# Kernel optimization log

Measured on AMD Instinct MI355X. Metric: run time of the kernel, lower is better.

The kernel has to match this reference:

```python
import jax, jax.numpy as jnp
import numpy as np

N, E = 100000, 1600000
IN, HID, OUT = 128, 64, 64
BN_EPS = 1e-5


def setup_inputs() -> dict:
    key = jax.random.key(0)
    ks = jax.random.split(key, 6)
    x = jax.random.normal(ks[0], (N, IN), dtype=jnp.float32)
    edge_index = jax.random.randint(ks[1], (2, E), 0, N, dtype=jnp.int32)
    W1 = jax.random.normal(ks[2], (IN, HID), dtype=jnp.float32) / np.sqrt(IN).astype(np.float32)
    b1 = jnp.zeros((HID,), jnp.float32)
    bn_weight = jnp.ones((HID,), jnp.float32)
    bn_bias = jnp.zeros((HID,), jnp.float32)
    W2 = jax.random.normal(ks[3], (HID, OUT), dtype=jnp.float32) / np.sqrt(HID).astype(np.float32)
    b2 = jnp.zeros((OUT,), jnp.float32)
    return {"x": x, "edge_index": edge_index, "W1": W1, "b1": b1,
            "bn_weight": bn_weight, "bn_bias": bn_bias, "W2": W2, "b2": b2}


def _gcn_conv(x, W, b, src, dst, deg_inv_sqrt):
    # PyG GCNConv: linear first, then symmetric-normalized aggregation with self-loops.
    h = x @ W                                        # [N, out]
    norm = deg_inv_sqrt[src] * deg_inv_sqrt[dst]     # [E]
    agg = jax.ops.segment_sum(h[src] * norm[:, None], dst, num_segments=h.shape[0])
    # self-loop contribution: norm = 1/deg
    agg = agg + h * (deg_inv_sqrt * deg_inv_sqrt)[:, None]
    return agg + b


def reference(x, edge_index, W1, b1, bn_weight, bn_bias, W2, b2):
    src, dst = edge_index[0], edge_index[1]
    # degree including self-loop (GCNConv add_self_loops=True, edge_weight=1)
    deg = jax.ops.segment_sum(jnp.ones((E,), x.dtype), dst, num_segments=N) + 1.0
    deg_inv_sqrt = jax.lax.rsqrt(deg)
    h = _gcn_conv(x, W1, b1, src, dst, deg_inv_sqrt)
    # BatchNorm1d (training-mode batch statistics, biased variance)
    mean = jnp.mean(h, axis=0)
    var = jnp.var(h, axis=0)
    h = (h - mean) * jax.lax.rsqrt(var + BN_EPS) * bn_weight + bn_bias
    h = jax.nn.relu(h)
    # dropout: inference mode (identity)
    return _gcn_conv(h, W2, b2, src, dst, deg_inv_sqrt)
```

## Files before the change

### kernel.cpp

```cpp
#include <hip/hip_runtime.h>

#define N_NODES 100000
#define E_EDGES 1600000
#define IN_F    128
#define HID_F   64
#define OUT_F   64
#define BN_EPS  1e-5f
#define NBUK    391
#define CHUNK   6250
#define NGBLK   3125
#define NMBLK   1563

typedef __bf16 bf16x8 __attribute__((ext_vector_type(8)));
typedef float  f32x4  __attribute__((ext_vector_type(4)));

__device__ __forceinline__ float bflo(unsigned int u) { return __uint_as_float(u << 16); }
__device__ __forceinline__ float bfhi(unsigned int u) { return __uint_as_float(u & 0xFFFF0000u); }
__device__ __forceinline__ unsigned int pack2bf(float a, float b) {
    unsigned int ua = __float_as_uint(a), ub = __float_as_uint(b);
    ua = (ua + 0x7fffu + ((ua >> 16) & 1u)) >> 16;
    ub = (ub + 0x7fffu + ((ub >> 16) & 1u)) >> 16;
    return ua | (ub << 16);
}
__device__ __forceinline__ unsigned short bf1(float a) {
    unsigned int ua = __float_as_uint(a);
    return (unsigned short)((ua + 0x7fffu + ((ua >> 16) & 1u)) >> 16);
}
#define ADD8(A, u)                                           \
    do {                                                     \
        A[0] += bflo((u).x); A[1] += bfhi((u).x);            \
        A[2] += bflo((u).y); A[3] += bfhi((u).y);            \
        A[4] += bflo((u).z); A[5] += bfhi((u).z);            \
        A[6] += bflo((u).w); A[7] += bfhi((u).w);            \
    } while (0)

__global__ __launch_bounds__(512) void k_chist(const int* __restrict__ dstv,
                                               int* __restrict__ histbuf) {
    __shared__ int h[NBUK];
    const int tid = threadIdx.x;
    const int e0 = blockIdx.x * CHUNK;
    for (int b = tid; b < NBUK; b += 512) h[b] = 0;
    __syncthreads();
    for (int t = tid; t < CHUNK; t += 512)
        atomicAdd(&h[dstv[e0 + t] >> 8], 1);
    __syncthreads();
    for (int b = tid; b < NBUK; b += 512)
        histbuf[blockIdx.x * NBUK + b] = h[b];
}

__global__ __launch_bounds__(512) void k_cscan(const int* __restrict__ histbuf,
                                               int* __restrict__ coff,
                                               int* __restrict__ ccur) {
    __shared__ int sh[512];
    const int tid = threadIdx.x;
    int v = 0;
    if (tid < NBUK)
        for (int b = 0; b < 256; ++b) v += histbuf[b * NBUK + tid];
    sh[tid] = v;
    __syncthreads();
    for (int off = 1; off < 512; off <<= 1) {
        int t = (tid >= off) ? sh[tid - off] : 0;
        __syncthreads();
        sh[tid] += t;
        __syncthreads();
    }
    int excl = sh[tid] - v;
    if (tid < NBUK) { coff[tid] = excl; ccur[tid] = excl; }
    if (tid == 0) coff[NBUK] = E_EDGES;
}

__global__ __launch_bounds__(512) void k_bucket(const int* __restrict__ srcv,
                                                const int* __restrict__ dstv,
                                                int* __restrict__ ccur,
                                                unsigned int* __restrict__ aux) {
    __shared__ int dl[CHUNK];
    __shared__ int hist[NBUK], base[NBUK], lcur[NBUK];
    const int tid = threadIdx.x;
    const int e0 = blockIdx.x * CHUNK;
    for (int b = tid; b < NBUK; b += 512) hist[b] = 0;
    __syncthreads();
    for (int t = tid; t < CHUNK; t += 512) {
        int d = dstv[e0 + t];
        dl[t] = d;
        atomicAdd(&hist[d >> 8], 1);
    }
    __syncthreads();
    for (int b = tid; b < NBUK; b += 512) {
        int h = hist[b];
        if (h) base[b] = atomicAdd(&ccur[b], h);
        lcur[b] = 0;
    }
    __syncthreads();
    for (int t = tid; t < CHUNK; t += 512) {
        int d = dl[t];
        int b = d >> 8;
        int off = atomicAdd(&lcur[b], 1);
        aux[base[b] + off] = ((unsigned int)srcv[e0 + t] << 8) | (unsigned int)(d & 255);
    }
}

__global__ __launch_bounds__(256) void k_csrnode(const int* __restrict__ coff,
                                                 const unsigned int* __restrict__ aux,
                                                 int* __restrict__ rowptr,
                                                 float* __restrict__ dis,
                                                 int* __restrict__ csr_src) {
    __shared__ int c0[256], sc[256], cur[256];
    const int tid = threadIdx.x;
    const int n0 = blockIdx.x * 256;
    const int nn = min(256, N_NODES - n0);
    const int estart = coff[blockIdx.x];
    const int eend   = coff[blockIdx.x + 1];
    c0[tid] = 0;
    __syncthreads();
    for (int e = estart + tid; e < eend; e += 256)
        atomicAdd(&c0[aux[e] & 255], 1);
    __syncthreads();
    int v = c0[tid];
    sc[tid] = v;
    __syncthreads();
    for (int off = 1; off < 256; off <<= 1) {
        int t = (tid >= off) ? sc[tid - off] : 0;
        __syncthreads();
        sc[tid] += t;
        __syncthreads();
    }
    int excl = sc[tid] - v;
    if (tid < nn) {
        int p = estart + excl;
        rowptr[n0 + tid] = p;
        cur[tid] = p;
        dis[n0 + tid] = rsqrtf((float)v + 1.0f);
    }
    if (blockIdx.x == NBUK - 1 && tid == 0) rowptr[N_NODES] = E_EDGES;
    __syncthreads();
    for (int e = estart + tid; e < eend; e += 256) {
        unsigned int u = aux[e];
        int pos = atomicAdd(&cur[u & 255], 1);
        csr_src[pos] = (int)(u >> 8);
    }
}

__global__ __launch_bounds__(256) void k_gemm1(const float* __restrict__ x,
                                               const float* __restrict__ W1,
                                               const float* __restrict__ dis,
                                               unsigned short* __restrict__ hs1) {
    __shared__ unsigned short Asb[64 * 136];
    __shared__ unsigned short Btb[64 * 136];
    __shared__ unsigned short Cc[64 * 72];
    __shared__ float disS[64];
    const int tid = threadIdx.x;
    const int r0 = blockIdx.x * 64;

    if (tid < 64) disS[tid] = (r0 + tid < N_NODES) ? dis[r0 + tid] : 0.f;

    const float4* x4 = (const float4*)x;
#pragma unroll
    for (int p = 0; p < 4; ++p) {
        int idx8 = p * 256 + tid;
        int row = idx8 >> 4, c8 = idx8 & 15;
        float4 v0 = make_float4(0.f, 0.f, 0.f, 0.f), v1 = v0;
        if (r0 + row < N_NODES) {
            v0 = x4[(size_t)(r0 + row) * 32 + c8 * 2];
            v1 = x4[(size_t)(r0 + row) * 32 + c8 * 2 + 1];
        }
        uint4 u;
        u.x = pack2bf(v0.x, v0.y); u.y = pack2bf(v0.z, v0.w);
        u.z = pack2bf(v1.x, v1.y); u.w = pack2bf(v1.z, v1.w);
        *(uint4*)&Asb[row * 136 + c8 * 8] = u;
    }
    for (int idx = tid; idx < IN_F * HID_F; idx += 256) {
        int k = idx >> 6, n = idx & 63;
        Btb[n * 136 + k] = bf1(W1[idx]);
    }
    __syncthreads();

    const int wv = tid >> 6, lane = tid & 63;
    const int m = lane & 15, quad = lane >> 4;
    const int arow = wv * 16 + m;
    f32x4 acc[4] = {};
#pragma unroll
    for (int ks = 0; ks < 4; ++ks) {
        int k0 = ks * 32 + quad * 8;
        bf16x8 af = *(const bf16x8*)&Asb[arow * 136 + k0];
#pragma unroll
        for (int c = 0; c < 4; ++c) {
            bf16x8 bfr = *(const bf16x8*)&Btb[(c * 16 + m) * 136 + k0];
            acc[c] = __builtin_amdgcn_mfma_f32_16x16x32_bf16(af, bfr, acc[c], 0, 0, 0);
        }
    }
#pragma unroll
    for (int c = 0; c < 4; ++c)
#pragma unroll
        for (int r = 0; r < 4; ++r) {
            int rl = wv * 16 + quad * 4 + r;
            Cc[rl * 72 + c * 16 + m] = bf1(acc[c][r] * disS[rl]);
        }
    __syncthreads();
#pragma unroll
    for (int p = 0; p < 2; ++p) {
        int idx = p * 256 + tid;
        int row = idx >> 3, c8 = idx & 7;
        if (r0 + row < N_NODES)
            *(uint4*)&hs1[(size_t)(r0 + row) * 64 + c8 * 8] = *(uint4*)&Cc[row * 72 + c8 * 8];
    }
}

__global__ __launch_bounds__(256) void k_gather1(const int* __restrict__ rowptr,
                                                 const int* __restrict__ csr_src,
                                                 const unsigned short* __restrict__ hsb,
                                                 const float* __restrict__ dis,
                                                 const float* __restrict__ b1,
                                                 unsigned short* __restrict__ aggb,
                                                 float* __restrict__ partials) {
    const int tid = threadIdx.x;
    const int g = tid >> 3, q = tid & 7;
    const int n = blockIdx.x * 32 + g;
    const uint4* __restrict__ hs16 = (const uint4*)hsb;

    const int start = rowptr[n], end = rowptr[n + 1];
    float A0[8] = {}, A1[8] = {}, A2[8] = {}, A3[8] = {};
    {
        uint4 u = hs16[(size_t)n * 8 + q];
        ADD8(A0, u);
    }
    int i = start;
    for (; i + 7 < end; i += 8) {
        int s0 = csr_src[i + 0], s1 = csr_src[i + 1];
        int s2 = csr_src[i + 2], s3 = csr_src[i + 3];
        int s4 = csr_src[i + 4], s5 = csr_src[i + 5];
        int s6 = csr_src[i + 6], s7 = csr_src[i + 7];
        uint4 u0 = hs16[(size_t)s0 * 8 + q];
        uint4 u1 = hs16[(size_t)s1 * 8 + q];
        uint4 u2 = hs16[(size_t)s2 * 8 + q];
        uint4 u3 = hs16[(size_t)s3 * 8 + q];
        uint4 u4 = hs16[(size_t)s4 * 8 + q];
        uint4 u5 = hs16[(size_t)s5 * 8 + q];
        uint4 u6 = hs16[(size_t)s6 * 8 + q];
        uint4 u7 = hs16[(size_t)s7 * 8 + q];
        ADD8(A0, u0); ADD8(A1, u1); ADD8(A2, u2); ADD8(A3, u3);
        ADD8(A0, u4); ADD8(A1, u5); ADD8(A2, u6); ADD8(A3, u7);
    }
    if (i + 3 < end) {
        int s0 = csr_src[i + 0], s1 = csr_src[i + 1];
        int s2 = csr_src[i + 2], s3 = csr_src[i + 3];
        uint4 u0 = hs16[(size_t)s0 * 8 + q];
        uint4 u1 = hs16[(size_t)s1 * 8 + q];
        uint4 u2 = hs16[(size_t)s2 * 8 + q];
        uint4 u3 = hs16[(size_t)s3 * 8 + q];
        ADD8(A0, u0); ADD8(A1, u1); ADD8(A2, u2); ADD8(A3, u3);
        i += 4;
    }
    for (; i < end; ++i) {
        uint4 u = hs16[(size_t)csr_src[i] * 8 + q];
        ADD8(A0, u);
    }
    const float d = dis[n];
    const float4 blo = ((const float4*)b1)[q * 2];
    const float4 bhi = ((const float4*)b1)[q * 2 + 1];
    float o[8];
    o[0] = fmaf(d, A0[0] + A1[0] + A2[0] + A3[0], blo.x);
    o[1] = fmaf(d, A0[1] + A1[1] + A2[1] + A3[1], blo.y);
    o[2] = fmaf(d, A0[2] + A1[2] + A2[2] + A3[2], blo.z);
    o[3] = fmaf(d, A0[3] + A1[3] + A2[3] + A3[3], blo.w);
    o[4] = fmaf(d, A0[4] + A1[4] + A2[4] + A3[4], bhi.x);
    o[5] = fmaf(d, A0[5] + A1[5] + A2[5] + A3[5], bhi.y);
    o[6] = fmaf(d, A0[6] + A1[6] + A2[6] + A3[6], bhi.z);
    o[7] = fmaf(d, A0[7] + A1[7] + A2[7] + A3[7], bhi.w);
    uint4 ob;
    ob.x = pack2bf(o[0], o[1]); ob.y = pack2bf(o[2], o[3]);
    ob.z = pack2bf(o[4], o[5]); ob.w = pack2bf(o[6], o[7]);
    ((uint4*)aggb)[(size_t)n * 8 + q] = ob;

    __shared__ float4 redA[256], redB[256];
    redA[tid] = make_float4(o[0], o[1], o[2], o[3]);
    redB[tid] = make_float4(o[4], o[5], o[6], o[7]);
    __syncthreads();
    for (int s = 128; s >= 8; s >>= 1) {
        if (tid < s) {
            redA[tid].x += redA[tid + s].x; redA[tid].y += redA[tid + s].y;
            redA[tid].z += redA[tid + s].z; redA[tid].w += redA[tid + s].w;
            redB[tid].x += redB[tid + s].x; redB[tid].y += redB[tid + s].y;
            redB[tid].z += redB[tid + s].z; redB[tid].w += redB[tid + s].w;
        }
        __syncthreads();
    }
    float4* pr = (float4*)(partials + (size_t)blockIdx.x * 128);
    if (tid < 8) { pr[tid * 2] = redA[tid]; pr[tid * 2 + 1] = redB[tid]; }
    __syncthreads();
    redA[tid] = make_float4(o[0] * o[0], o[1] * o[1], o[2] * o[2], o[3] * o[3]);
    redB[tid] = make_float4(o[4] * o[4], o[5] * o[5], o[6] * o[6], o[7] * o[7]);
    __syncthreads();
    for (int s = 128; s >= 8; s >>= 1) {
        if (tid < s) {
            redA[tid].x += redA[tid + s].x; redA[tid].y += redA[tid + s].y;
            redA[tid].z += redA[tid + s].z; redA[tid].w += redA[tid + s].w;
            redB[tid].x += redB[tid + s].x; redB[tid].y += redB[tid + s].y;
            redB[tid].z += redB[tid + s].z; redB[tid].w += redB[tid + s].w;
        }
        __syncthreads();
    }
    if (tid < 8) { pr[16 + tid * 2] = redA[tid]; pr[16 + tid * 2 + 1] = redB[tid]; }
}

__global__ __launch_bounds__(256) void k_bnfinal(const float* __restrict__ partials,
                                                 float* __restrict__ bnstats) {
    const int c = blockIdx.x;
    const int tid = threadIdx.x;
    float s = 0.f;
    for (int r = tid; r < NGBLK; r += 256)
        s += partials[(size_t)r * 128 + c];
    __shared__ float sh[256];
    sh[tid] = s;
    __syncthreads();
    for (int st = 128; st > 0; st >>= 1) {
        if (tid < st) sh[tid] += sh[tid + st];
        __syncthreads();
    }
    if (tid == 0) bnstats[c] = sh[0];
}

__global__ __launch_bounds__(256) void k_gemm2(const unsigned short* __restrict__ aggb,
                                               const float* __restrict__ W2,
                                               const float* __restrict__ dis,
                                               const float* __restrict__ bnw,
                                               const float* __restrict__ bnb,
                                               const float* __restrict__ bnstats,
                                               unsigned short* __restrict__ hs2) {
    __shared__ unsigned short Ab[64 * 72];
    __shared__ unsigned short Bt2[64 * 72];
    __shared__ unsigned short Cc[64 * 72];
    __shared__ float scale_s[64], shift_s[64], disS[64];
    const int tid = threadIdx.x;
    const int r0 = blockIdx.x * 64;

    if (tid < 64) {
        const float invN = 1.0f / (float)N_NODES;
        float mean = bnstats[tid] * invN;
        float var  = bnstats[64 + tid] * invN - mean * mean;
        float sc   = bnw[tid] * rsqrtf(var + BN_EPS);
        scale_s[tid] = sc;
        shift_s[tid] = fmaf(-mean, sc, bnb[tid]);
        disS[tid] = (r0 + tid < N_NODES) ? dis[r0 + tid] : 0.f;
    }
    for (int idx = tid; idx < HID_F * OUT_F; idx += 256) {
        int k = idx >> 6, n = idx & 63;
        Bt2[n * 72 + k] = bf1(W2[idx]);
    }
    __syncthreads();

    const uint4* a16 = (const uint4*)aggb;
#pragma unroll
    for (int p = 0; p < 2; ++p) {
        int idx = p * 256 + tid;
        int row = idx >> 3, q = idx & 7;
        uint4 u = make_uint4(0, 0, 0, 0);
        if (r0 + row < N_NODES) u = a16[(size_t)(r0 + row) * 8 + q];
        int k0 = q * 8;
        float v[8];
        v[0] = bflo(u.x); v[1] = bfhi(u.x); v[2] = bflo(u.y); v[3] = bfhi(u.y);
        v[4] = bflo(u.z); v[5] = bfhi(u.z); v[6] = bflo(u.w); v[7] = bfhi(u.w);
        uint4 o;
        float w0 = fmaxf(fmaf(v[0], scale_s[k0 + 0], shift_s[k0 + 0]), 0.f);
        float w1 = fmaxf(fmaf(v[1], scale_s[k0 + 1], shift_s[k0 + 1]), 0.f);
        float w2 = fmaxf(fmaf(v[2], scale_s[k0 + 2], shift_s[k0 + 2]), 0.f);
        float w3 = fmaxf(fmaf(v[3], scale_s[k0 + 3], shift_s[k0 + 3]), 0.f);
        float w4 = fmaxf(fmaf(v[4], scale_s[k0 + 4], shift_s[k0 + 4]), 0.f);
        float w5 = fmaxf(fmaf(v[5], scale_s[k0 + 5], shift_s[k0 + 5]), 0.f);
        float w6 = fmaxf(fmaf(v[6], scale_s[k0 + 6], shift_s[k0 + 6]), 0.f);
        float w7 = fmaxf(fmaf(v[7], scale_s[k0 + 7], shift_s[k0 + 7]), 0.f);
        o.x = pack2bf(w0, w1); o.y = pack2bf(w2, w3);
        o.z = pack2bf(w4, w5); o.w = pack2bf(w6, w7);
        *(uint4*)&Ab[row * 72 + q * 8] = o;
    }
    __syncthreads();

    const int wv = tid >> 6, lane = tid & 63;
    const int m = lane & 15, quad = lane >> 4;
    const int arow = wv * 16 + m;
    f32x4 acc[4] = {};
#pragma unroll
    for (int ks = 0; ks < 2; ++ks) {
        int k0 = ks * 32 + quad * 8;
        bf16x8 af = *(const bf16x8*)&Ab[arow * 72 + k0];
#pragma unroll
        for (int c = 0; c < 4; ++c) {
            bf16x8 bfr = *(const bf16x8*)&Bt2[(c * 16 + m) * 72 + k0];
            acc[c] = __builtin_amdgcn_mfma_f32_16x16x32_bf16(af, bfr, acc[c], 0, 0, 0);
        }
    }
#pragma unroll
    for (int c = 0; c < 4; ++c)
#pragma unroll
        for (int r = 0; r < 4; ++r) {
            int rl = wv * 16 + quad * 4 + r;
            Cc[rl * 72 + c * 16 + m] = bf1(acc[c][r] * disS[rl]);
        }
    __syncthreads();
#pragma unroll
    for (int p = 0; p < 2; ++p) {
        int idx = p * 256 + tid;
        int row = idx >> 3, c8 = idx & 7;
        if (r0 + row < N_NODES)
            *(uint4*)&hs2[(size_t)(r0 + row) * 64 + c8 * 8] = *(uint4*)&Cc[row * 72 + c8 * 8];
    }
}

__global__ __launch_bounds__(256) void k_gather2(const int* __restrict__ rowptr,
                                                 const int* __restrict__ csr_src,
                                                 const unsigned short* __restrict__ hsb,
                                                 const float* __restrict__ dis,
                                                 const float* __restrict__ b2,
                                                 float* __restrict__ out) {
    const int tid = threadIdx.x;
    const int g = tid >> 3, q = tid & 7;
    const int n = blockIdx.x * 32 + g;
    const uint4* __restrict__ hs16 = (const uint4*)hsb;

    const int start = rowptr[n], end = rowptr[n + 1];
    float A0[8] = {}, A1[8] = {}, A2[8] = {}, A3[8] = {};
    {
        uint4 u = hs16[(size_t)n * 8 + q];
        ADD8(A0, u);
    }
    int i = start;
    for (; i + 7 < end; i += 8) {
        int s0 = csr_src[i + 0], s1 = csr_src[i + 1];
        int s2 = csr_src[i + 2], s3 = csr_src[i + 3];
        int s4 = csr_src[i + 4], s5 = csr_src[i + 5];
        int s6 = csr_src[i + 6], s7 = csr_src[i + 7];
        uint4 u0 = hs16[(size_t)s0 * 8 + q];
        uint4 u1 = hs16[(size_t)s1 * 8 + q];
        uint4 u2 = hs16[(size_t)s2 * 8 + q];
        uint4 u3 = hs16[(size_t)s3 * 8 + q];
        uint4 u4 = hs16[(size_t)s4 * 8 + q];
        uint4 u5 = hs16[(size_t)s5 * 8 + q];
        uint4 u6 = hs16[(size_t)s6 * 8 + q];
        uint4 u7 = hs16[(size_t)s7 * 8 + q];
        ADD8(A0, u0); ADD8(A1, u1); ADD8(A2, u2); ADD8(A3, u3);
        ADD8(A0, u4); ADD8(A1, u5); ADD8(A2, u6); ADD8(A3, u7);
    }
    if (i + 3 < end) {
        int s0 = csr_src[i + 0], s1 = csr_src[i + 1];
        int s2 = csr_src[i + 2], s3 = csr_src[i + 3];
        uint4 u0 = hs16[(size_t)s0 * 8 + q];
        uint4 u1 = hs16[(size_t)s1 * 8 + q];
        uint4 u2 = hs16[(size_t)s2 * 8 + q];
        uint4 u3 = hs16[(size_t)s3 * 8 + q];
        ADD8(A0, u0); ADD8(A1, u1); ADD8(A2, u2); ADD8(A3, u3);
        i += 4;
    }
    for (; i < end; ++i) {
        uint4 u = hs16[(size_t)csr_src[i] * 8 + q];
        ADD8(A0, u);
    }
    const float d = dis[n];
    const float4 blo = ((const float4*)b2)[q * 2];
    const float4 bhi = ((const float4*)b2)[q * 2 + 1];
    float4 o0, o1;
    o0.x = fmaf(d, A0[0] + A1[0] + A2[0] + A3[0], blo.x);
    o0.y = fmaf(d, A0[1] + A1[1] + A2[1] + A3[1], blo.y);
    o0.z = fmaf(d, A0[2] + A1[2] + A2[2] + A3[2], blo.z);
    o0.w = fmaf(d, A0[3] + A1[3] + A2[3] + A3[3], blo.w);
    o1.x = fmaf(d, A0[4] + A1[4] + A2[4] + A3[4], bhi.x);
    o1.y = fmaf(d, A0[5] + A1[5] + A2[5] + A3[5], bhi.y);
    o1.z = fmaf(d, A0[6] + A1[6] + A2[6] + A3[6], bhi.z);
    o1.w = fmaf(d, A0[7] + A1[7] + A2[7] + A3[7], bhi.w);
    float4* op = (float4*)(out + (size_t)n * OUT_F + q * 8);
    op[0] = o0;
    op[1] = o1;
}

extern "C" void kernel_launch(void* const* d_in, const int* in_sizes, int n_in,
                              void* d_out, int out_size, void* d_ws, size_t ws_size,
                              hipStream_t stream) {
    const float* x   = (const float*)d_in[0];
    const int*   ei  = (const int*)d_in[1];
    const float* W1  = (const float*)d_in[2];
    const float* b1  = (const float*)d_in[3];
    const float* bnw = (const float*)d_in[4];
    const float* bnb = (const float*)d_in[5];
    const float* W2  = (const float*)d_in[6];
    const float* b2  = (const float*)d_in[7];
    float* out = (float*)d_out;

    float* ws = (float*)d_ws;
    float*        dis     = ws;
    int*          rowptr  = (int*)(ws + 100352);
    int*          coff    = (int*)(ws + 200960);
    int*          ccur    = (int*)(ws + 201472);
    float*        bnstats = ws + 201984;
    int*          histbuf = (int*)(ws + 202112);
    int*          csr_src = (int*)(ws + 302464);
    float*        bufA    = ws + 1902464;
    float*        bufB    = bufA + (size_t)N_NODES * HID_F;
    unsigned int*   aux  = (unsigned int*)bufA;
    unsigned short* hsb  = (unsigned short*)bufA;
    unsigned short* aggb = (unsigned short*)bufB;
    float* partials = out;

    const int* srcv = ei;
    const int* dstv = ei + E_EDGES;

    k_chist  <<<256, 512, 0, stream>>>(dstv, histbuf);
    k_cscan  <<<1, 512, 0, stream>>>(histbuf, coff, ccur);
    k_bucket <<<256, 512, 0, stream>>>(srcv, dstv, ccur, aux);
    k_csrnode<<<NBUK, 256, 0, stream>>>(coff, aux, rowptr, dis, csr_src);

    k_gemm1  <<<NMBLK, 256, 0, stream>>>(x, W1, dis, hsb);
    k_gather1<<<NGBLK, 256, 0, stream>>>(rowptr, csr_src, hsb, dis, b1, aggb, partials);
    k_bnfinal<<<128, 256, 0, stream>>>(partials, bnstats);
    k_gemm2  <<<NMBLK, 256, 0, stream>>>(aggb, W2, dis, bnw, bnb, bnstats, hsb);
    k_gather2<<<NGBLK, 256, 0, stream>>>(rowptr, csr_src, hsb, dis, b2, out);
}
```

Measured before the change: 252.0 us.

## Parallelize bucket scan and process four nodes per group in gather kernels

The single-block column-sum scan is replaced by a per-bucket parallel scan over the 256 chunk histograms plus a small scan of bucket totals. This yields deterministic per-chunk write offsets, so the bucketing kernel drops its second shared-memory histogram pass and its global atomics. The gather kernels now use 64-thread blocks, with each 8-lane group handling four nodes in sequence, and BN partial statistics are accumulated in registers before the block reduction. The cost is less parallelism per block in the gathers and one extra kernel launch.

New measurement: 239.8 us. 4.9% less time.

```diff
diff --git a/kernel.cpp b/kernel.cpp
--- a/kernel.cpp
+++ b/kernel.cpp
@@ -48,14 +48,28 @@
         histbuf[blockIdx.x * NBUK + b] = h[b];
 }
 
-__global__ __launch_bounds__(512) void k_cscan(const int* __restrict__ histbuf,
-                                               int* __restrict__ coff,
-                                               int* __restrict__ ccur) {
+__global__ __launch_bounds__(256) void k_cscan1(int* __restrict__ histbuf,
+                                                int* __restrict__ btot) {
+    __shared__ int sh[256];
+    const int bkt = blockIdx.x, tid = threadIdx.x;
+    int v = histbuf[tid * NBUK + bkt];
+    sh[tid] = v;
+    __syncthreads();
+    for (int off = 1; off < 256; off <<= 1) {
+        int t = (tid >= off) ? sh[tid - off] : 0;
+        __syncthreads();
+        sh[tid] += t;
+        __syncthreads();
+    }
+    histbuf[tid * NBUK + bkt] = sh[tid] - v;
+    if (tid == 255) btot[bkt] = sh[255];
+}
+
+__global__ __launch_bounds__(512) void k_cscan2(const int* __restrict__ btot,
+                                                int* __restrict__ coff) {
     __shared__ int sh[512];
     const int tid = threadIdx.x;
-    int v = 0;
-    if (tid < NBUK)
-        for (int b = 0; b < 256; ++b) v += histbuf[b * NBUK + tid];
+    int v = (tid < NBUK) ? btot[tid] : 0;
     sh[tid] = v;
     __syncthreads();
     for (int off = 1; off < 512; off <<= 1) {
@@ -64,38 +78,26 @@
         sh[tid] += t;
         __syncthreads();
     }
-    int excl = sh[tid] - v;
-    if (tid < NBUK) { coff[tid] = excl; ccur[tid] = excl; }
+    if (tid < NBUK) coff[tid] = sh[tid] - v;
     if (tid == 0) coff[NBUK] = E_EDGES;
 }
 
 __global__ __launch_bounds__(512) void k_bucket(const int* __restrict__ srcv,
                                                 const int* __restrict__ dstv,
-                                                int* __restrict__ ccur,
+                                                const int* __restrict__ histbuf,
+                                                const int* __restrict__ coff,
                                                 unsigned int* __restrict__ aux) {
-    __shared__ int dl[CHUNK];
-    __shared__ int hist[NBUK], base[NBUK], lcur[NBUK];
+    __shared__ int cur[NBUK];
     const int tid = threadIdx.x;
     const int e0 = blockIdx.x * CHUNK;
-    for (int b = tid; b < NBUK; b += 512) hist[b] = 0;
+    for (int i = tid; i < NBUK; i += 512)
+        cur[i] = histbuf[blockIdx.x * NBUK + i] + coff[i];
     __syncthreads();
     for (int t = tid; t < CHUNK; t += 512) {
         int d = dstv[e0 + t];
-        dl[t] = d;
-        atomicAdd(&hist[d >> 8], 1);
-    }
-    __syncthreads();
-    for (int b = tid; b < NBUK; b += 512) {
-        int h = hist[b];
-        if (h) base[b] = atomicAdd(&ccur[b], h);
-        lcur[b] = 0;
-    }
-    __syncthreads();
-    for (int t = tid; t < CHUNK; t += 512) {
-        int d = dl[t];
-        int b = d >> 8;
-        int off = atomicAdd(&lcur[b], 1);
-        aux[base[b] + off] = ((unsigned int)srcv[e0 + t] << 8) | (unsigned int)(d & 255);
+        int s = srcv[e0 + t];
+        int pos = atomicAdd(&cur[d >> 8], 1);
+        aux[pos] = ((unsigned int)s << 8) | (unsigned int)(d & 255);
     }
 }
 
@@ -205,77 +207,88 @@
     }
 }
 
-__global__ __launch_bounds__(256) void k_gather1(const int* __restrict__ rowptr,
-                                                 const int* __restrict__ csr_src,
-                                                 const unsigned short* __restrict__ hsb,
-                                                 const float* __restrict__ dis,
-                                                 const float* __restrict__ b1,
-                                                 unsigned short* __restrict__ aggb,
-                                                 float* __restrict__ partials) {
+__global__ __launch_bounds__(64) void k_gather1(const int* __restrict__ rowptr,
+                                                const int* __restrict__ csr_src,
+                                                const unsigned short* __restrict__ hsb,
+                                                const float* __restrict__ dis,
+                                                const float* __restrict__ b1,
+                                                unsigned short* __restrict__ aggb,
+                                                float* __restrict__ partials) {
     const int tid = threadIdx.x;
     const int g = tid >> 3, q = tid & 7;
-    const int n = blockIdx.x * 32 + g;
     const uint4* __restrict__ hs16 = (const uint4*)hsb;
-
-    const int start = rowptr[n], end = rowptr[n + 1];
-    float A0[8] = {}, A1[8] = {}, A2[8] = {}, A3[8] = {};
-    {
-        uint4 u = hs16[(size_t)n * 8 + q];
-        ADD8(A0, u);
-    }
-    int i = start;
-    for (; i + 7 < end; i += 8) {
-        int s0 = csr_src[i + 0], s1 = csr_src[i + 1];
-        int s2 = csr_src[i + 2], s3 = csr_src[i + 3];
-        int s4 = csr_src[i + 4], s5 = csr_src[i + 5];
-        int s6 = csr_src[i + 6], s7 = csr_src[i + 7];
-        uint4 u0 = hs16[(size_t)s0 * 8 + q];
-        uint4 u1 = hs16[(size_t)s1 * 8 + q];
-        uint4 u2 = hs16[(size_t)s2 * 8 + q];
-        uint4 u3 = hs16[(size_t)s3 * 8 + q];
-        uint4 u4 = hs16[(size_t)s4 * 8 + q];
-        uint4 u5 = hs16[(size_t)s5 * 8 + q];
-        uint4 u6 = hs16[(size_t)s6 * 8 + q];
-        uint4 u7 = hs16[(size_t)s7 * 8 + q];
-        ADD8(A0, u0); ADD8(A1, u1); ADD8(A2, u2); ADD8(A3, u3);
-        ADD8(A0, u4); ADD8(A1, u5); ADD8(A2, u6); ADD8(A3, u7);
-    }
-    if (i + 3 < end) {
-        int s0 = csr_src[i + 0], s1 = csr_src[i + 1];
-        int s2 = csr_src[i + 2], s3 = csr_src[i + 3];
-        uint4 u0 = hs16[(size_t)s0 * 8 + q];
-        uint4 u1 = hs16[(size_t)s1 * 8 + q];
-        uint4 u2 = hs16[(size_t)s2 * 8 + q];
-        uint4 u3 = hs16[(size_t)s3 * 8 + q];
-        ADD8(A0, u0); ADD8(A1, u1); ADD8(A2, u2); ADD8(A3, u3);
-        i += 4;
-    }
-    for (; i < end; ++i) {
-        uint4 u = hs16[(size_t)csr_src[i] * 8 + q];
-        ADD8(A0, u);
-    }
-    const float d = dis[n];
     const float4 blo = ((const float4*)b1)[q * 2];
     const float4 bhi = ((const float4*)b1)[q * 2 + 1];
-    float o[8];
-    o[0] = fmaf(d, A0[0] + A1[0] + A2[0] + A3[0], blo.x);
-    o[1] = fmaf(d, A0[1] + A1[1] + A2[1] + A3[1], blo.y);
-    o[2] = fmaf(d, A0[2] + A1[2] + A2[2] + A3[2], blo.z);
-    o[3] = fmaf(d, A0[3] + A1[3] + A2[3] + A3[3], blo.w);
-    o[4] = fmaf(d, A0[4] + A1[4] + A2[4] + A3[4], bhi.x);
-    o[5] = fmaf(d, A0[5] + A1[5] + A2[5] + A3[5], bhi.y);
-    o[6] = fmaf(d, A0[6] + A1[6] + A2[6] + A3[6], bhi.z);
-    o[7] = fmaf(d, A0[7] + A1[7] + A2[7] + A3[7], bhi.w);
-    uint4 ob;
-    ob.x = pack2bf(o[0], o[1]); ob.y = pack2bf(o[2], o[3]);
-    ob.z = pack2bf(o[4], o[5]); ob.w = pack2bf(o[6], o[7]);
-    ((uint4*)aggb)[(size_t)n * 8 + q] = ob;
-
-    __shared__ float4 redA[256], redB[256];
-    redA[tid] = make_float4(o[0], o[1], o[2], o[3]);
-    redB[tid] = make_float4(o[4], o[5], o[6], o[7]);
-    __syncthreads();
-    for (int s = 128; s >= 8; s >>= 1) {
+
+    float bsA[4] = {}, bsB[4] = {}, bqA[4] = {}, bqB[4] = {};
+
+#pragma unroll
+    for (int jj = 0; jj < 4; ++jj) {
+        const int n = blockIdx.x * 32 + jj * 8 + g;
+        const int start = rowptr[n], end = rowptr[n + 1];
+        float A0[8] = {}, A1[8] = {}, A2[8] = {}, A3[8] = {};
+        {
+            uint4 u = hs16[(size_t)n * 8 + q];
+            ADD8(A0, u);
+        }
+        int i = start;
+        for (; i + 7 < end; i += 8) {
+            int s0 = csr_src[i + 0], s1 = csr_src[i + 1];
+            int s2 = csr_src[i + 2], s3 = csr_src[i + 3];
+            int s4 = csr_src[i + 4], s5 = csr_src[i + 5];
+            int s6 = csr_src[i + 6], s7 = csr_src[i + 7];
+            uint4 u0 = hs16[(size_t)s0 * 8 + q];
+            uint4 u1 = hs16[(size_t)s1 * 8 + q];
+            uint4 u2 = hs16[(size_t)s2 * 8 + q];
+            uint4 u3 = hs16[(size_t)s3 * 8 + q];
+            uint4 u4 = hs16[(size_t)s4 * 8 + q];
+            uint4 u5 = hs16[(size_t)s5 * 8 + q];
+            uint4 u6 = hs16[(size_t)s6 * 8 + q];
+            uint4 u7 = hs16[(size_t)s7 * 8 + q];
+            ADD8(A0, u0); ADD8(A1, u1); ADD8(A2, u2); ADD8(A3, u3);
+            ADD8(A0, u4); ADD8(A1, u5); ADD8(A2, u6); ADD8(A3, u7);
+        }
+        if (i + 3 < end) {
+            int s0 = csr_src[i + 0], s1 = csr_src[i + 1];
+            int s2 = csr_src[i + 2], s3 = csr_src[i + 3];
+            uint4 u0 = hs16[(size_t)s0 * 8 + q];
+            uint4 u1 = hs16[(size_t)s1 * 8 + q];
+            uint4 u2 = hs16[(size_t)s2 * 8 + q];
+            uint4 u3 = hs16[(size_t)s3 * 8 + q];
+            ADD8(A0, u0); ADD8(A1, u1); ADD8(A2, u2); ADD8(A3, u3);
+            i += 4;
+        }
+        for (; i < end; ++i) {
+            uint4 u = hs16[(size_t)csr_src[i] * 8 + q];
+            ADD8(A0, u);
+        }
+        const float d = dis[n];
+        float o[8];
+        o[0] = fmaf(d, A0[0] + A1[0] + A2[0] + A3[0], blo.x);
+        o[1] = fmaf(d, A0[1] + A1[1] + A2[1] + A3[1], blo.y);
+        o[2] = fmaf(d, A0[2] + A1[2] + A2[2] + A3[2], blo.z);
+        o[3] = fmaf(d, A0[3] + A1[3] + A2[3] + A3[3], blo.w);
+        o[4] = fmaf(d, A0[4] + A1[4] + A2[4] + A3[4], bhi.x);
+        o[5] = fmaf(d, A0[5] + A1[5] + A2[5] + A3[5], bhi.y);
+        o[6] = fmaf(d, A0[6] + A1[6] + A2[6] + A3[6], bhi.z);
+        o[7] = fmaf(d, A0[7] + A1[7] + A2[7] + A3[7], bhi.w);
+        uint4 ob;
+        ob.x = pack2bf(o[0], o[1]); ob.y = pack2bf(o[2], o[3]);
+        ob.z = pack2bf(o[4], o[5]); ob.w = pack2bf(o[6], o[7]);
+        ((uint4*)aggb)[(size_t)n * 8 + q] = ob;
+#pragma unroll
+        for (int k = 0; k < 4; ++k) {
+            bsA[k] += o[k];     bsB[k] += o[4 + k];
+            bqA[k] = fmaf(o[k], o[k], bqA[k]);
+            bqB[k] = fmaf(o[4 + k], o[4 + k], bqB[k]);
+        }
+    }
+
+    __shared__ float4 redA[64], redB[64];
+    redA[tid] = make_float4(bsA[0], bsA[1], bsA[2], bsA[3]);
+    redB[tid] = make_float4(bsB[0], bsB[1], bsB[2], bsB[3]);
+    __syncthreads();
+    for (int s = 32; s >= 8; s >>= 1) {
         if (tid < s) {
             redA[tid].x += redA[tid + s].x; redA[tid].y += redA[tid + s].y;
             redA[tid].z += redA[tid + s].z; redA[tid].w += redA[tid + s].w;
@@ -287,10 +300,10 @@
     float4* pr = (float4*)(partials + (size_t)blockIdx.x * 128);
     if (tid < 8) { pr[tid * 2] = redA[tid]; pr[tid * 2 + 1] = redB[tid]; }
     __syncthreads();
-    redA[tid] = make_float4(o[0] * o[0], o[1] * o[1], o[2] * o[2], o[3] * o[3]);
-    redB[tid] = make_float4(o[4] * o[4], o[5] * o[5], o[6] * o[6], o[7] * o[7]);
-    __syncthreads();
-    for (int s = 128; s >= 8; s >>= 1) {
+    redA[tid] = make_float4(bqA[0], bqA[1], bqA[2], bqA[3]);
+    redB[tid] = make_float4(bqB[0], bqB[1], bqB[2], bqB[3]);
+    __syncthreads();
+    for (int s = 32; s >= 8; s >>= 1) {
         if (tid < s) {
             redA[tid].x += redA[tid + s].x; redA[tid].y += redA[tid + s].y;
             redA[tid].z += redA[tid + s].z; redA[tid].w += redA[tid + s].w;
@@ -405,69 +418,72 @@
     }
 }
 
-__global__ __launch_bounds__(256) void k_gather2(const int* __restrict__ rowptr,
-                                                 const int* __restrict__ csr_src,
-                                                 const unsigned short* __restrict__ hsb,
-                                                 const float* __restrict__ dis,
-                                                 const float* __restrict__ b2,
-                                                 float* __restrict__ out) {
+__global__ __launch_bounds__(64) void k_gather2(const int* __restrict__ rowptr,
+                                                const int* __restrict__ csr_src,
+                                                const unsigned short* __restrict__ hsb,
+                                                const float* __restrict__ dis,
+                                                const float* __restrict__ b2,
+                                                float* __restrict__ out) {
     const int tid = threadIdx.x;
     const int g = tid >> 3, q = tid & 7;
-    const int n = blockIdx.x * 32 + g;
     const uint4* __restrict__ hs16 = (const uint4*)hsb;
-
-    const int start = rowptr[n], end = rowptr[n + 1];
-    float A0[8] = {}, A1[8] = {}, A2[8] = {}, A3[8] = {};
-    {
-        uint4 u = hs16[(size_t)n * 8 + q];
-        ADD8(A0, u);
-    }
-    int i = start;
-    for (; i + 7 < end; i += 8) {
-        int s0 = csr_src[i + 0], s1 = csr_src[i + 1];
-        int s2 = csr_src[i + 2], s3 = csr_src[i + 3];
-        int s4 = csr_src[i + 4], s5 = csr_src[i + 5];
-        int s6 = csr_src[i + 6], s7 = csr_src[i + 7];
-        uint4 u0 = hs16[(size_t)s0 * 8 + q];
-        uint4 u1 = hs16[(size_t)s1 * 8 + q];
-        uint4 u2 = hs16[(size_t)s2 * 8 + q];
-        uint4 u3 = hs16[(size_t)s3 * 8 + q];
-        uint4 u4 = hs16[(size_t)s4 * 8 + q];
-        uint4 u5 = hs16[(size_t)s5 * 8 + q];
-        uint4 u6 = hs16[(size_t)s6 * 8 + q];
-        uint4 u7 = hs16[(size_t)s7 * 8 + q];
-        ADD8(A0, u0); ADD8(A1, u1); ADD8(A2, u2); ADD8(A3, u3);
-        ADD8(A0, u4); ADD8(A1, u5); ADD8(A2, u6); ADD8(A3, u7);
-    }
-    if (i + 3 < end) {
-        int s0 = csr_src[i + 0], s1 = csr_src[i + 1];
-        int s2 = csr_src[i + 2], s3 = csr_src[i + 3];
-        uint4 u0 = hs16[(size_t)s0 * 8 + q];
-        uint4 u1 = hs16[(size_t)s1 * 8 + q];
-        uint4 u2 = hs16[(size_t)s2 * 8 + q];
-        uint4 u3 = hs16[(size_t)s3 * 8 + q];
-        ADD8(A0, u0); ADD8(A1, u1); ADD8(A2, u2); ADD8(A3, u3);
-        i += 4;
-    }
-    for (; i < end; ++i) {
-        uint4 u = hs16[(size_t)csr_src[i] * 8 + q];
-        ADD8(A0, u);
-    }
-    const float d = dis[n];
     const float4 blo = ((const float4*)b2)[q * 2];
     const float4 bhi = ((const float4*)b2)[q * 2 + 1];
-    float4 o0, o1;
-    o0.x = fmaf(d, A0[0] + A1[0] + A2[0] + A3[0], blo.x);
-    o0.y = fmaf(d, A0[1] + A1[1] + A2[1] + A3[1], blo.y);
-    o0.z = fmaf(d, A0[2] + A1[2] + A2[2] + A3[2], blo.z);
-    o0.w = fmaf(d, A0[3] + A1[3] + A2[3] + A3[3], blo.w);
-    o1.x = fmaf(d, A0[4] + A1[4] + A2[4] + A3[4], bhi.x);
-    o1.y = fmaf(d, A0[5] + A1[5] + A2[5] + A3[5], bhi.y);
-    o1.z = fmaf(d, A0[6] + A1[6] + A2[6] + A3[6], bhi.z);
-    o1.w = fmaf(d, A0[7] + A1[7] + A2[7] + A3[7], bhi.w);
-    float4* op = (float4*)(out + (size_t)n * OUT_F + q * 8);
-    op[0] = o0;
-    op[1] = o1;
+
+#pragma unroll
+    for (int jj = 0; jj < 4; ++jj) {
+        const int n = blockIdx.x * 32 + jj * 8 + g;
+        const int start = rowptr[n], end = rowptr[n + 1];
+        float A0[8] = {}, A1[8] = {}, A2[8] = {}, A3[8] = {};
+        {
+            uint4 u = hs16[(size_t)n * 8 + q];
+            ADD8(A0, u);
+        }
+        int i = start;
+        for (; i + 7 < end; i += 8) {
+            int s0 = csr_src[i + 0], s1 = csr_src[i + 1];
+            int s2 = csr_src[i + 2], s3 = csr_src[i + 3];
+            int s4 = csr_src[i + 4], s5 = csr_src[i + 5];
+            int s6 = csr_src[i + 6], s7 = csr_src[i + 7];
+            uint4 u0 = hs16[(size_t)s0 * 8 + q];
+            uint4 u1 = hs16[(size_t)s1 * 8 + q];
+            uint4 u2 = hs16[(size_t)s2 * 8 + q];
+            uint4 u3 = hs16[(size_t)s3 * 8 + q];
+            uint4 u4 = hs16[(size_t)s4 * 8 + q];
+            uint4 u5 = hs16[(size_t)s5 * 8 + q];
+            uint4 u6 = hs16[(size_t)s6 * 8 + q];
+            uint4 u7 = hs16[(size_t)s7 * 8 + q];
+            ADD8(A0, u0); ADD8(A1, u1); ADD8(A2, u2); ADD8(A3, u3);
+            ADD8(A0, u4); ADD8(A1, u5); ADD8(A2, u6); ADD8(A3, u7);
+        }
+        if (i + 3 < end) {
+            int s0 = csr_src[i + 0], s1 = csr_src[i + 1];
+            int s2 = csr_src[i + 2], s3 = csr_src[i + 3];
+            uint4 u0 = hs16[(size_t)s0 * 8 + q];
+            uint4 u1 = hs16[(size_t)s1 * 8 + q];
+            uint4 u2 = hs16[(size_t)s2 * 8 + q];
+            uint4 u3 = hs16[(size_t)s3 * 8 + q];
+            ADD8(A0, u0); ADD8(A1, u1); ADD8(A2, u2); ADD8(A3, u3);
+            i += 4;
+        }
+        for (; i < end; ++i) {
+            uint4 u = hs16[(size_t)csr_src[i] * 8 + q];
+            ADD8(A0, u);
+        }
+        const float d = dis[n];
+        float4 o0, o1;
+        o0.x = fmaf(d, A0[0] + A1[0] + A2[0] + A3[0], blo.x);
+        o0.y = fmaf(d, A0[1] + A1[1] + A2[1] + A3[1], blo.y);
+        o0.z = fmaf(d, A0[2] + A1[2] + A2[2] + A3[2], blo.z);
+        o0.w = fmaf(d, A0[3] + A1[3] + A2[3] + A3[3], blo.w);
+        o1.x = fmaf(d, A0[4] + A1[4] + A2[4] + A3[4], bhi.x);
+        o1.y = fmaf(d, A0[5] + A1[5] + A2[5] + A3[5], bhi.y);
+        o1.z = fmaf(d, A0[6] + A1[6] + A2[6] + A3[6], bhi.z);
+        o1.w = fmaf(d, A0[7] + A1[7] + A2[7] + A3[7], bhi.w);
+        float4* op = (float4*)(out + (size_t)n * OUT_F + q * 8);
+        op[0] = o0;
+        op[1] = o1;
+    }
 }
 
 extern "C" void kernel_launch(void* const* d_in, const int* in_sizes, int n_in,
@@ -487,7 +503,7 @@
     float*        dis     = ws;
     int*          rowptr  = (int*)(ws + 100352);
     int*          coff    = (int*)(ws + 200960);
-    int*          ccur    = (int*)(ws + 201472);
+    int*          btot    = (int*)(ws + 201472);
     float*        bnstats = ws + 201984;
     int*          histbuf = (int*)(ws + 202112);
     int*          csr_src = (int*)(ws + 302464);
@@ -502,13 +518,14 @@
     const int* dstv = ei + E_EDGES;
 
     k_chist  <<<256, 512, 0, stream>>>(dstv, histbuf);
-    k_cscan  <<<1, 512, 0, stream>>>(histbuf, coff, ccur);
-    k_bucket <<<256, 512, 0, stream>>>(srcv, dstv, ccur, aux);
+    k_cscan1 <<<NBUK, 256, 0, stream>>>(histbuf, btot);
+    k_cscan2 <<<1, 512, 0, stream>>>(btot, coff);
+    k_bucket <<<256, 512, 0, stream>>>(srcv, dstv, histbuf, coff, aux);
     k_csrnode<<<NBUK, 256, 0, stream>>>(coff, aux, rowptr, dis, csr_src);
 
     k_gemm1  <<<NMBLK, 256, 0, stream>>>(x, W1, dis, hsb);
-    k_gather1<<<NGBLK, 256, 0, stream>>>(rowptr, csr_src, hsb, dis, b1, aggb, partials);
+    k_gather1<<<NGBLK, 64, 0, stream>>>(rowptr, csr_src, hsb, dis, b1, aggb, partials);
     k_bnfinal<<<128, 256, 0, stream>>>(partials, bnstats);
     k_gemm2  <<<NMBLK, 256, 0, stream>>>(aggb, W2, dis, bnw, bnb, bnstats, hsb);
-    k_gather2<<<NGBLK, 256, 0, stream>>>(rowptr, csr_src, hsb, dis, b2, out);
-}
+    k_gather2<<<NGBLK, 64, 0, stream>>>(rowptr, csr_src, hsb, dis, b2, out);
+}
```
